# Kernel optimization log

Measured on AMD Instinct MI355X. Metric: run time of the kernel, lower is better.

The kernel has to match this reference:

```python
import jax, jax.numpy as jnp
import numpy as np

EPS = 1e-8  # torch F.cosine_similarity eps
QK_DIM = 16


def conv2d(x, w, b=None):
    # x: [N,C,H,W], w: [O,I,kh,kw]
    y = jax.lax.conv_general_dilated(x, w, (1, 1), 'SAME',
                                     dimension_numbers=('NCHW', 'OIHW', 'NCHW'))
    return y if b is None else y + b[None, :, None, None]


def setup_inputs() -> dict:
    key = jax.random.key(0)
    ks = jax.random.split(key, 32)
    N, H, W = 5, 256, 256
    c_vox, c_feat, c_det, c_sem = 8, 64, 8, 32
    c_total = c_vox + c_feat + c_det  # 80
    r = lambda k, sh: jax.random.normal(k, sh, dtype=jnp.float32)
    p = lambda k, sh: 0.02 * jax.random.normal(k, sh, dtype=jnp.float32)
    return {
        # BEV inputs
        'ego_vox': r(ks[0], (1, c_vox, H, W)),
        'ego_feat': r(ks[1], (1, c_feat, H, W)),
        'ego_det': r(ks[2], (1, c_det, H, W)),
        'collab_vox': r(ks[3], (N, c_vox, H, W)),
        'collab_feat': r(ks[4], (N, c_feat, H, W)),
        'collab_det': r(ks[5], (N, c_det, H, W)),
        # QueryGenerator (1x1 conv, no bias)
        'q_w': p(ks[6], (QK_DIM, c_feat, 1, 1)),
        # Channel_Request_Attention shared MLP (1x1 convs, no bias, ratio=16)
        'ch_w1': p(ks[7], (c_feat // 16, c_feat)),
        'ch_w2': p(ks[8], (c_feat, c_feat // 16)),
        # KeyGenerator (1x1 convs, no bias)
        'k_w1': p(ks[9], (QK_DIM, c_vox, 1, 1)),
        'k_w2': p(ks[10], (QK_DIM, c_feat, 1, 1)),
        'k_w3': p(ks[11], (QK_DIM, c_det, 1, 1)),
        # AttentionGenerator: spatial branch
        'sp_w1': p(ks[12], (64, c_total, 3, 3)), 'sp_b1': jnp.zeros((64,), jnp.float32),
        'sp_w2': p(ks[13], (1, 64, 1, 1)), 'sp_b2': jnp.zeros((1,), jnp.float32),
        # AttentionGenerator: granularity branch (linears)
        'gr_w1': p(ks[14], (32, c_total)), 'gr_b1': jnp.zeros((32,), jnp.float32),
        'gr_w2': p(ks[15], (3, 32)), 'gr_b2': jnp.zeros((3,), jnp.float32),
        # AttentionGenerator: semantic branch
        'se_w1': p(ks[16], (128, c_feat, 3, 3)), 'se_b1': jnp.zeros((128,), jnp.float32),
        'se_w2': p(ks[17], (c_sem, 128, 1, 1)), 'se_b2': jnp.zeros((c_sem,), jnp.float32),
    }


def _forward(ego_vox, ego_feat, ego_det, collab_vox, collab_feat, collab_det,
             q_w, ch_w1, ch_w2, k_w1, k_w2, k_w3,
             sp_w1, sp_b1, sp_w2, sp_b2, gr_w1, gr_b1, gr_w2, gr_b2,
             se_w1, se_b1, se_w2, se_b2):
    N = collab_vox.shape[0]

    # ---- _calculate_contribution(ref=ego broadcast to N, contrib=collab) ----
    # padded cosine sims reduce to slice-dot / (||slice|| * ||ref_full||)
    sq = lambda t: jnp.sum(t * t, axis=1)                      # [*,H,W]
    ref_norm = jnp.sqrt(sq(ego_vox) + sq(ego_feat) + sq(ego_det))  # [1,H,W]
    denom_ref = jnp.maximum(ref_norm, EPS)

    def sim(contrib, ego_part):
        dot = jnp.sum(contrib * ego_part, axis=1)              # [N,H,W]
        n = jnp.maximum(jnp.sqrt(sq(contrib)), EPS)
        return dot / (n * denom_ref)

    contribution = jnp.stack(
        [sim(collab_vox, ego_vox), sim(collab_feat, ego_feat), sim(collab_det, ego_det)],
        axis=1)                                                 # [N,3,H,W]
    contribution = (contribution + 1.0) * 0.5

    # ---- QueryGenerator / KeyGenerator cross-agent attention ----
    q = conv2d(ego_feat, q_w)                                   # [1,16,H,W]
    k1 = conv2d(collab_vox, k_w1)                               # [N,16,H,W]
    k2 = conv2d(collab_feat, k_w2)
    k3 = conv2d(collab_det, k_w3)
    scale = 1.0 / np.sqrt(QK_DIM).astype(np.float32)
    scores = jnp.stack([jnp.sum(q * k, axis=1) for k in (k1, k2, k3)],
                       axis=1) * scale                          # [N,3,H,W]
    qk_attn = jax.nn.softmax(scores, axis=1)

    # ---- Channel_Request_Attention on ego feat (note: max_pool is also avg pool in source) ----
    pooled = jnp.mean(ego_feat, axis=(2, 3))                    # [1,64]
    m = jax.nn.relu(pooled @ ch_w1.T) @ ch_w2.T                 # [1,64]
    channel_attn = jax.nn.sigmoid(m + m)[:, :, None, None]      # [1,64,1,1]

    # ---- AttentionGenerator over collaborators ----
    full = jnp.concatenate([collab_vox, collab_feat, collab_det], axis=1)  # [N,80,H,W]
    spatial_attn = jax.nn.sigmoid(
        conv2d(jax.nn.relu(conv2d(full, sp_w1, sp_b1)), sp_w2, sp_b2))     # [N,1,H,W]
    pooled_full = jnp.mean(full, axis=(2, 3))                   # [N,80]
    gran_attn = jax.nn.softmax(
        jax.nn.relu(pooled_full @ gr_w1.T + gr_b1) @ gr_w2.T + gr_b2,
        axis=-1)[:, :, None, None]                              # [N,3,1,1]
    sem_attn = conv2d(jax.nn.relu(conv2d(collab_feat, se_w1, se_b1)),
                      se_w2, se_b2)                             # [N,32,H,W]

    return (contribution, qk_attn, spatial_attn, gran_attn, sem_attn, channel_attn)


def reference(ego_vox, ego_feat, ego_det, collab_vox, collab_feat, collab_det,
              q_w, ch_w1, ch_w2, k_w1, k_w2, k_w3,
              sp_w1, sp_b1, sp_w2, sp_b2, gr_w1, gr_b1, gr_w2, gr_b2,
              se_w1, se_b1, se_w2, se_b2):
    return _forward(ego_vox, ego_feat, ego_det, collab_vox, collab_feat, collab_det,
                    q_w, ch_w1, ch_w2, k_w1, k_w2, k_w3,
                    sp_w1, sp_b1, sp_w2, sp_b2, gr_w1, gr_b1, gr_w2, gr_b2,
                    se_w1, se_b1, se_w2, se_b2)
```

## Files before the change

kernel.cpp:

```cpp
#include <hip/hip_runtime.h>
#include <math.h>

#define HW 65536
#define NAG 5
#define EPSF 1e-8f

typedef __attribute__((ext_vector_type(8))) short short8;
typedef __attribute__((ext_vector_type(4))) float f32x4;

__device__ __forceinline__ unsigned short f2bf(float f) {
    union { float f; unsigned int u; } v; v.f = f;
    unsigned int r = v.u + 0x7FFF + ((v.u >> 16) & 1);
    return (unsigned short)(r >> 16);
}

__device__ __forceinline__ void gload_lds16(const unsigned short* g, unsigned short* l) {
    __builtin_amdgcn_global_load_lds(
        (__attribute__((address_space(1))) void*)(g),
        (__attribute__((address_space(3))) void*)(l),
        16, 0, 0);
}

__device__ __forceinline__ int swz1280(int orig) {
    return (orig & 7) * 160 + (orig >> 3);
}

__device__ __forceinline__ f32x4 MF(short8 a, short8 b, f32x4 c) {
    return __builtin_amdgcn_mfma_f32_16x16x32_bf16(a, b, c, 0, 0, 0);
}


__global__ __launch_bounds__(256) void k_transpose(
    const float* __restrict__ q_w, const float* __restrict__ k_w1,
    const float* __restrict__ k_w2, const float* __restrict__ k_w3,
    float* __restrict__ qwT, float* __restrict__ kw1T,
    float* __restrict__ kw2T, float* __restrict__ kw3T)
{
    int i = blockIdx.x * 256 + threadIdx.x;
    if (i < 1024)  { int o = i / 64,  c = i % 64;  qwT[c * 16 + o] = q_w[i];
                                                   kw2T[c * 16 + o] = k_w2[i]; }
    if (i < 128)   { int o = i / 8,   c = i % 8;   kw1T[c * 16 + o] = k_w1[i];
                                                   kw3T[c * 16 + o] = k_w3[i]; }
}

__global__ __launch_bounds__(256) void k_prep(
    const float* __restrict__ se_w1, const float* __restrict__ se_w2,
    const float* __restrict__ sp_w1,
    unsigned short* __restrict__ wbf, unsigned short* __restrict__ w2bf,
    unsigned short* __restrict__ wspf, unsigned short* __restrict__ wspv)
{
    int i = blockIdx.x * 256 + threadIdx.x;
    if (i < 73728) {
        int c = i & 63, mid = (i >> 6) & 127, tap = i >> 13;
        wbf[i] = f2bf(se_w1[(mid * 64 + c) * 9 + tap]);
    }
    if (i < 4096) w2bf[i] = f2bf(se_w2[i]);
    if (i < 36864) {
        int c = i & 63, mid = (i >> 6) & 63, tap = i >> 12;
        wspf[i] = f2bf(sp_w1[(mid * 80 + 8 + c) * 9 + tap]);
    }
    if (i < 18432) {
        int c = i & 31, mid = (i >> 5) & 63, tap = i >> 11;
        float v = 0.f;
        if (c < 8)       v = sp_w1[(mid * 80 + c) * 9 + tap];
        else if (c < 16) v = sp_w1[(mid * 80 + 64 + c) * 9 + tap];
        wspv[i] = f2bf(v);
    }
}

__global__ __launch_bounds__(256) void k_prep_nhwc(
    const float* __restrict__ ego_feat,
    const float* __restrict__ collab_vox, const float* __restrict__ collab_feat,
    const float* __restrict__ collab_det,
    unsigned short* __restrict__ featNHWC, unsigned short* __restrict__ vdNHWC,
    float* __restrict__ partials)
{
    __shared__ float lds_f[64 * 65];
    const int y = blockIdx.x, n = blockIdx.y;
    const int t = threadIdx.x;
    const bool ego = (n == 5);
    const float* featsrc = ego ? ego_feat : collab_feat + (size_t)n * 64 * HW;

    float psum = 0.f;
    const int c_ld = t >> 2, q0 = t & 3;
    for (int chunk = 0; chunk < 4; ++chunk) {
        const int x0c = chunk * 64;
        __syncthreads();
#pragma unroll
        for (int q = q0; q < 16; q += 4) {
            float4 v = *(const float4*)&featsrc[(size_t)c_ld * HW + y * 256 + x0c + q * 4];
            lds_f[c_ld * 65 + q * 4 + 0] = v.x;
            lds_f[c_ld * 65 + q * 4 + 1] = v.y;
            lds_f[c_ld * 65 + q * 4 + 2] = v.z;
            lds_f[c_ld * 65 + q * 4 + 3] = v.w;
            psum += (v.x + v.y) + (v.z + v.w);
        }
        __syncthreads();
        if (!ego) {
#pragma unroll
            for (int half = 0; half < 2; ++half) {
                int g = t & 7, xl = (t >> 3) + half * 32;
                int x = x0c + xl;
                int cg = g ^ (x & 7);
                unsigned short pk[8];
#pragma unroll
                for (int i = 0; i < 8; ++i)
                    pk[i] = f2bf(lds_f[(cg * 8 + i) * 65 + xl]);
                *(short8*)&featNHWC[(((size_t)n * 256 + y) * 256 + x) * 64 + g * 8] =
                    *(const short8*)pk;
            }
        }
    }
    psum += __shfl_xor(psum, 1, 64);
    psum += __shfl_xor(psum, 2, 64);
    if (q0 == 0) {
        int row = ego ? c_ld : 64 + n * 80 + 8 + c_ld;
        partials[row * 256 + y] = psum;
    }
    if (ego) return;

    float psv = 0.f;
    const int c2 = t >> 4, q2 = t & 15;
    const float* vdsrc = (c2 < 8) ? collab_vox + ((size_t)n * 8 + c2) * HW
                                  : collab_det + ((size_t)n * 8 + (c2 - 8)) * HW;
    for (int chunk = 0; chunk < 4; ++chunk) {
        const int x0c = chunk * 64;
        __syncthreads();
        {
            float4 v = *(const float4*)&vdsrc[y * 256 + x0c + q2 * 4];
            lds_f[c2 * 65 + q2 * 4 + 0] = v.x;
            lds_f[c2 * 65 + q2 * 4 + 1] = v.y;
            lds_f[c2 * 65 + q2 * 4 + 2] = v.z;
            lds_f[c2 * 65 + q2 * 4 + 3] = v.w;
            psv += (v.x + v.y) + (v.z + v.w);
        }
        __syncthreads();
        {
            int g = t & 3, xl = t >> 2;
            int x = x0c + xl;
            int cg = g ^ (x & 3);
            unsigned short pk[8];
#pragma unroll
            for (int i = 0; i < 8; ++i) {
                int cc = cg * 8 + i;
                pk[i] = (cc < 16) ? f2bf(lds_f[cc * 65 + xl]) : (unsigned short)0;
            }
            *(short8*)&vdNHWC[(((size_t)n * 256 + y) * 256 + x) * 32 + g * 8] =
                *(const short8*)pk;
        }
    }
    psv += __shfl_xor(psv, 1, 64);
    psv += __shfl_xor(psv, 2, 64);
    psv += __shfl_xor(psv, 4, 64);
    psv += __shfl_xor(psv, 8, 64);
    if (q2 == 0) {
        int row = 64 + n * 80 + (c2 < 8 ? c2 : c2 + 64);
        partials[row * 256 + y] = psv;
    }
}

__global__ __launch_bounds__(256) void k_pool2(
    const float* __restrict__ partials, float* __restrict__ pool)
{
    __shared__ float red[256];
    int r = blockIdx.x, t = threadIdx.x;
    red[t] = partials[r * 256 + t];
    __syncthreads();
    for (int s = 128; s > 0; s >>= 1) {
        if (t < s) red[t] += red[t + s];
        __syncthreads();
    }
    if (t == 0) pool[r] = red[0] * (1.f / HW);
}

__global__ __launch_bounds__(256) void k_contrib_qk(
    const float* __restrict__ ego_vox, const float* __restrict__ ego_feat,
    const float* __restrict__ ego_det,
    const float* __restrict__ collab_vox, const float* __restrict__ collab_feat,
    const float* __restrict__ collab_det,
    const float* __restrict__ qw, const float* __restrict__ kw1,
    const float* __restrict__ kw2, const float* __restrict__ kw3,
    float* __restrict__ out_contrib, float* __restrict__ out_qk)
{
    const int n = blockIdx.x >> 8;
    const int p = ((blockIdx.x & 255) << 8) | threadIdx.x;

    float q[16], k2[16];
#pragma unroll
    for (int o = 0; o < 16; o++) { q[o] = 0.f; k2[o] = 0.f; }
    float sq_ref = 0.f, dot_f = 0.f, sq_cf = 0.f;
#pragma unroll 4
    for (int c = 0; c < 64; c++) {
        float e = ego_feat[c * HW + p];
        float x = collab_feat[(n * 64 + c) * HW + p];
        sq_ref = fmaf(e, e, sq_ref);
        dot_f  = fmaf(x, e, dot_f);
        sq_cf  = fmaf(x, x, sq_cf);
#pragma unroll
        for (int o = 0; o < 16; o++) {
            q[o]  = fmaf(qw[c * 16 + o], e, q[o]);
            k2[o] = fmaf(kw2[c * 16 + o], x, k2[o]);
        }
    }
    float kx[16];
#pragma unroll
    for (int o = 0; o < 16; o++) kx[o] = 0.f;
    float dot_v = 0.f, sq_cv = 0.f;
#pragma unroll
    for (int c = 0; c < 8; c++) {
        float e = ego_vox[c * HW + p];
        float x = collab_vox[(n * 8 + c) * HW + p];
        sq_ref = fmaf(e, e, sq_ref);
        dot_v  = fmaf(x, e, dot_v);
        sq_cv  = fmaf(x, x, sq_cv);
#pragma unroll
        for (int o = 0; o < 16; o++)
            kx[o] = fmaf(kw1[c * 16 + o], x, kx[o]);
    }
    float s1 = 0.f;
#pragma unroll
    for (int o = 0; o < 16; o++) s1 = fmaf(q[o], kx[o], s1);
#pragma unroll
    for (int o = 0; o < 16; o++) kx[o] = 0.f;
    float dot_d = 0.f, sq_cd = 0.f;
#pragma unroll
    for (int c = 0; c < 8; c++) {
        float e = ego_det[c * HW + p];
        float x = collab_det[(n * 8 + c) * HW + p];
        sq_ref = fmaf(e, e, sq_ref);
        dot_d  = fmaf(x, e, dot_d);
        sq_cd  = fmaf(x, x, sq_cd);
#pragma unroll
        for (int o = 0; o < 16; o++)
            kx[o] = fmaf(kw3[c * 16 + o], x, kx[o]);
    }
    float s3 = 0.f, s2 = 0.f;
#pragma unroll
    for (int o = 0; o < 16; o++) { s3 = fmaf(q[o], kx[o], s3); s2 = fmaf(q[o], k2[o], s2); }

    float inv_ref = 1.f / fmaxf(sqrtf(sq_ref), EPSF);
    float simv = dot_v / fmaxf(sqrtf(sq_cv), EPSF) * inv_ref;
    float simf = dot_f / fmaxf(sqrtf(sq_cf), EPSF) * inv_ref;
    float simd_ = dot_d / fmaxf(sqrtf(sq_cd), EPSF) * inv_ref;
    out_contrib[(n * 3 + 0) * HW + p] = (simv + 1.f) * 0.5f;
    out_contrib[(n * 3 + 1) * HW + p] = (simf + 1.f) * 0.5f;
    out_contrib[(n * 3 + 2) * HW + p] = (simd_ + 1.f) * 0.5f;

    s1 *= 0.25f; s2 *= 0.25f; s3 *= 0.25f;
    float m = fmaxf(s1, fmaxf(s2, s3));
    float e1 = __expf(s1 - m), e2 = __expf(s2 - m), e3 = __expf(s3 - m);
    float inv = 1.f / (e1 + e2 + e3);
    out_qk[(n * 3 + 0) * HW + p] = e1 * inv;
    out_qk[(n * 3 + 1) * HW + p] = e2 * inv;
    out_qk[(n * 3 + 2) * HW + p] = e3 * inv;
}

__global__ __launch_bounds__(192) void k_mlps(
    const float* __restrict__ pool,
    const float* __restrict__ ch_w1, const float* __restrict__ ch_w2,
    const float* __restrict__ gr_w1, const float* __restrict__ gr_b1,
    const float* __restrict__ gr_w2, const float* __restrict__ gr_b2,
    float* __restrict__ out_gran, float* __restrict__ out_chan)
{
    __shared__ float h4[4], h32[5][32], logit[5][3];
    int t = threadIdx.x;
    if (t < 4) {
        float a = 0.f;
        for (int c = 0; c < 64; c++) a = fmaf(ch_w1[t * 64 + c], pool[c], a);
        h4[t] = fmaxf(a, 0.f);
    }
    if (t < 160) {
        int n = t >> 5, i = t & 31;
        float a = gr_b1[i];
        for (int c = 0; c < 80; c++) a = fmaf(gr_w1[i * 80 + c], pool[64 + n * 80 + c], a);
        h32[n][i] = fmaxf(a, 0.f);
    }
    __syncthreads();
    if (t < 64) {
        float m = 0.f;
#pragma unroll
        for (int j = 0; j < 4; j++) m = fmaf(ch_w2[t * 4 + j], h4[j], m);
        out_chan[t] = 1.f / (1.f + __expf(-2.f * m));
    }
    if (t < 15) {
        int n = t / 3, j = t % 3;
        float a = gr_b2[j];
#pragma unroll
        for (int i = 0; i < 32; i++) a = fmaf(gr_w2[j * 32 + i], h32[n][i], a);
        logit[n][j] = a;
    }
    __syncthreads();
    if (t < 5) {
        float a = logit[t][0], b = logit[t][1], c = logit[t][2];
        float m = fmaxf(a, fmaxf(b, c));
        float ea = __expf(a - m), eb = __expf(b - m), ec = __expf(c - m);
        float inv = 1.f / (ea + eb + ec);
        out_gran[t * 3 + 0] = ea * inv;
        out_gran[t * 3 + 1] = eb * inv;
        out_gran[t * 3 + 2] = ec * inv;
    }
}

__global__ __launch_bounds__(512, 4) void k_sem_nhwc(
    const unsigned short* __restrict__ featNHWC,
    const unsigned short* __restrict__ wbf,
    const unsigned short* __restrict__ w2bf,
    const float* __restrict__ se_b1, const float* __restrict__ se_b2,
    float* __restrict__ out_sem)
{
    __shared__ __align__(16) unsigned short smem[256 * 128];
    const int bid = swz1280((int)blockIdx.x);
    const int n = bid >> 8, rem = bid & 255;
    const int x0 = (rem & 3) << 6, y0 = (rem >> 2) << 2;
    const int tid = threadIdx.x, lane = tid & 63, w = tid >> 6;
    const int wr = w >> 1, wc = w & 1;
    const int l15 = lane & 15, lg = lane >> 4;
    const short8 z8 = {0, 0, 0, 0, 0, 0, 0, 0};

    if (y0 == 0)
        for (int i = tid; i < 528; i += 512) *(short8*)&smem[i * 8] = z8;
    if (y0 == 252)
        for (int i = tid; i < 528; i += 512) *(short8*)&smem[5 * 66 * 64 + i * 8] = z8;

    for (int idx = w; idx < 48; idx += 8) {
        int dy = idx >> 3, k = idx & 7, gy = y0 - 1 + dy;
        if ((unsigned)gy < 256u)
            gload_lds16(
                &featNHWC[(((size_t)n * 256 + gy) * 256 + x0 + k * 8 + (lane >> 3)) * 64 + (lane & 7) * 8],
                &smem[(dy * 66 + 1 + k * 8) * 64]);
    }
    if (tid < 96) {
        int dy = tid >> 4, rem2 = tid & 15, side = rem2 >> 3, c8 = rem2 & 7;
        int gy = y0 - 1 + dy, gx = side ? x0 + 64 : x0 - 1, col = side ? 65 : 0;
        short8 v = z8;
        if ((unsigned)gy < 256u && (unsigned)gx < 256u)
            v = *(const short8*)&featNHWC[(((size_t)n * 256 + gy) * 256 + gx) * 64 + c8 * 8];
        *(short8*)&smem[(dy * 66 + col) * 64 + c8 * 8] = v;
    }
    __syncthreads();

    const int midb = wc * 64 + l15;
    f32x4 acc[4][4] = {};
    short8 bc[4], bn[4];
#pragma unroll
    for (int nf = 0; nf < 4; ++nf)
        bc[nf] = *(const short8*)&wbf[(0 * 128 + midb + nf * 16) * 64 + lg * 8];

#pragma unroll 1
    for (int p = 0; p < 18; ++p) {
        const int tap = p >> 1, kc = p & 1;
        const int dyrow = tap / 3, dx = tap % 3;
        const int pn = (p < 17) ? p + 1 : 17;
        const int tapn = pn >> 1, kcn = pn & 1;
#pragma unroll
        for (int nf = 0; nf < 4; ++nf)
            bn[nf] = *(const short8*)&wbf[(tapn * 128 + midb + nf * 16) * 64 + kcn * 32 + lg * 8];
        const int c0 = kc * 32 + lg * 8;
        const int dyb = (wr + dyrow) * 66;
        short8 a[4];
#pragma unroll
        for (int mf = 0; mf < 4; ++mf) {
            int col = mf * 16 + l15 + dx;
            a[mf] = *(const short8*)&smem[(dyb + col) * 64 + (c0 ^ (((col + 7) & 7) << 3))];
        }
        __builtin_amdgcn_s_setprio(1);
#pragma unroll
        for (int mf = 0; mf < 4; ++mf)
#pragma unroll
            for (int nf = 0; nf < 4; ++nf)
                acc[mf][nf] = MF(a[mf], bc[nf], acc[mf][nf]);
        __builtin_amdgcn_s_setprio(0);
#pragma unroll
        for (int nf = 0; nf < 4; ++nf) bc[nf] = bn[nf];
    }
    __syncthreads();

#pragma unroll
    for (int nf = 0; nf < 4; ++nf) {
        int mid = wc * 64 + nf * 16 + l15;
        float b1 = se_b1[mid];
#pragma unroll
        for (int mf = 0; mf < 4; ++mf) {
            int mrow = wr * 64 + mf * 16 + lg * 4;
#pragma unroll
            for (int rr = 0; rr < 4; ++rr) {
                int m = mrow + rr;
                float v = fmaxf(acc[mf][nf][rr] + b1, 0.f);
                smem[m * 128 + (mid ^ ((m & 7) << 3))] = f2bf(v);
            }
        }
    }
    __syncthreads();

    f32x4 acc2[2][2] = {};
    const int pxb = w * 32;
#pragma unroll
    for (int kc = 0; kc < 4; ++kc) {
        const int k0 = kc * 32 + lg * 8;
        short8 a2[2], b2[2];
#pragma unroll
        for (int mf = 0; mf < 2; ++mf) {
            int m = pxb + mf * 16 + l15;
            a2[mf] = *(const short8*)&smem[m * 128 + (k0 ^ ((m & 7) << 3))];
        }
#pragma unroll
        for (int nf = 0; nf < 2; ++nf) {
            int j = nf * 16 + l15;
            b2[nf] = *(const short8*)&w2bf[j * 128 + k0];
        }
#pragma unroll
        for (int mf = 0; mf < 2; ++mf)
#pragma unroll
            for (int nf = 0; nf < 2; ++nf)
                acc2[mf][nf] = MF(a2[mf], b2[nf], acc2[mf][nf]);
    }
#pragma unroll
    for (int nf = 0; nf < 2; ++nf) {
        int j = nf * 16 + l15;
        float bj = se_b2[j];
#pragma unroll
        for (int mf = 0; mf < 2; ++mf) {
            int m = pxb + mf * 16 + lg * 4;
            int oy = m >> 6, x = m & 63;
            float4 v;
            v.x = acc2[mf][nf][0] + bj; v.y = acc2[mf][nf][1] + bj;
            v.z = acc2[mf][nf][2] + bj; v.w = acc2[mf][nf][3] + bj;
            *(float4*)&out_sem[(size_t)(n * 32 + j) * HW + (y0 + oy) * 256 + x0 + x] = v;
        }
    }
}

__global__ __launch_bounds__(512, 4) void k_spatial_nhwc(
    const unsigned short* __restrict__ featNHWC,
    const unsigned short* __restrict__ vdNHWC,
    const unsigned short* __restrict__ wspf,
    const unsigned short* __restrict__ wspv,
    const float* __restrict__ sp_b1, const float* __restrict__ sp_w2,
    const float* __restrict__ sp_b2,
    float* __restrict__ out_sp)
{
    __shared__ __align__(16) unsigned short sF[6 * 66 * 64];
    __shared__ __align__(16) unsigned short sV[6 * 66 * 32];
    const int bid = swz1280((int)blockIdx.x);
    const int n = bid >> 8, rem = bid & 255;
    const int x0 = (rem & 3) << 6, y0 = (rem >> 2) << 2;
    const int tid = threadIdx.x, lane = tid & 63, w = tid >> 6;
    const int l15 = lane & 15, lg = lane >> 4;
    const int wr = w >> 1, wc = w & 1;
    const short8 z8 = {0, 0, 0, 0, 0, 0, 0, 0};

    if (y0 == 0) {
        for (int i = tid; i < 528; i += 512) *(short8*)&sF[i * 8] = z8;
        for (int i = tid; i < 264; i += 512) *(short8*)&sV[i * 8] = z8;
    }
    if (y0 == 252) {
        for (int i = tid; i < 528; i += 512) *(short8*)&sF[5 * 66 * 64 + i * 8] = z8;
        for (int i = tid; i < 264; i += 512) *(short8*)&sV[5 * 66 * 32 + i * 8] = z8;
    }
    for (int idx = w; idx < 48; idx += 8) {
        int dy = idx >> 3, k = idx & 7, gy = y0 - 1 + dy;
        if ((unsigned)gy < 256u)
            gload_lds16(
                &featNHWC[(((size_t)n * 256 + gy) * 256 + x0 + k * 8 + (lane >> 3)) * 64 + (lane & 7) * 8],
                &sF[(dy * 66 + 1 + k * 8) * 64]);
    }
    for (int idx = w; idx < 24; idx += 8) {
        int dy = idx >> 2, k = idx & 3, gy = y0 - 1 + dy;
        if ((unsigned)gy < 256u)
            gload_lds16(
                &vdNHWC[(((size_t)n * 256 + gy) * 256 + x0 + k * 16 + (lane >> 2)) * 32 + (lane & 3) * 8],
                &sV[(dy * 66 + 1 + k * 16) * 32]);
    }
    if (tid < 96) {
        int dy = tid >> 4, rem2 = tid & 15, side = rem2 >> 3, c8 = rem2 & 7;
        int gy = y0 - 1 + dy, gx = side ? x0 + 64 : x0 - 1, col = side ? 65 : 0;
        short8 v = z8;
        if ((unsigned)gy < 256u && (unsigned)gx < 256u)
            v = *(const short8*)&featNHWC[(((size_t)n * 256 + gy) * 256 + gx) * 64 + c8 * 8];
        *(short8*)&sF[(dy * 66 + col) * 64 + c8 * 8] = v;
    } else if (tid < 144) {
        int t2 = tid - 96;
        int dy = t2 >> 3, rem2 = t2 & 7, side = rem2 >> 2, g4 = rem2 & 3;
        int gy = y0 - 1 + dy, gx = side ? x0 + 64 : x0 - 1, col = side ? 65 : 0;
        short8 v = z8;
        if ((unsigned)gy < 256u && (unsigned)gx < 256u)
            v = *(const short8*)&vdNHWC[(((size_t)n * 256 + gy) * 256 + gx) * 32 + g4 * 8];
        *(short8*)&sV[(dy * 66 + col) * 32 + g4 * 8] = v;
    }
    __syncthreads();

    f32x4 acc[4][2] = {};
    const int mid0 = wc * 32 + l15, mid1 = wc * 32 + 16 + l15;

    short8 bc0 = *(const short8*)&wspf[(0 * 64 + mid0) * 64 + lg * 8];
    short8 bc1 = *(const short8*)&wspf[(0 * 64 + mid1) * 64 + lg * 8];
#pragma unroll 1
    for (int p = 0; p < 18; ++p) {
        const int tap = p >> 1, kc = p & 1;
        const int dyrow = tap / 3, dx = tap % 3;
        const int pn = (p < 17) ? p + 1 : 17;
        const int tapn = pn >> 1, kcn = pn & 1;
        short8 bn0 = *(const short8*)&wspf[(tapn * 64 + mid0) * 64 + kcn * 32 + lg * 8];
        short8 bn1 = *(const short8*)&wspf[(tapn * 64 + mid1) * 64 + kcn * 32 + lg * 8];
        const int c0 = kc * 32 + lg * 8;
        const int dyb = (wr + dyrow) * 66;
        short8 a[4];
#pragma unroll
        for (int mf = 0; mf < 4; ++mf) {
            int col = mf * 16 + l15 + dx;
            a[mf] = *(const short8*)&sF[(dyb + col) * 64 + (c0 ^ (((col + 7) & 7) << 3))];
        }
        __builtin_amdgcn_s_setprio(1);
#pragma unroll
        for (int mf = 0; mf < 4; ++mf) {
            acc[mf][0] = MF(a[mf], bc0, acc[mf][0]);
            acc[mf][1] = MF(a[mf], bc1, acc[mf][1]);
        }
        __builtin_amdgcn_s_setprio(0);
        bc0 = bn0; bc1 = bn1;
    }

    const int c0v = lg * 8;
    short8 vc0 = *(const short8*)&wspv[(0 * 64 + mid0) * 32 + c0v];
    short8 vc1 = *(const short8*)&wspv[(0 * 64 + mid1) * 32 + c0v];
#pragma unroll 1
    for (int tap = 0; tap < 9; ++tap) {
        const int dyrow = tap / 3, dx = tap % 3;
        const int tapn = (tap < 8) ? tap + 1 : 8;
        short8 vn0 = *(const short8*)&wspv[(tapn * 64 + mid0) * 32 + c0v];
        short8 vn1 = *(const short8*)&wspv[(tapn * 64 + mid1) * 32 + c0v];
        const int dyb = (wr + dyrow) * 66;
        short8 a[4];
#pragma unroll
        for (int mf = 0; mf < 4; ++mf) {
            int col = mf * 16 + l15 + dx;
            a[mf] = *(const short8*)&sV[(dyb + col) * 32 + (c0v ^ (((col + 3) & 3) << 3))];
        }
        __builtin_amdgcn_s_setprio(1);
#pragma unroll
        for (int mf = 0; mf < 4; ++mf) {
            acc[mf][0] = MF(a[mf], vc0, acc[mf][0]);
            acc[mf][1] = MF(a[mf], vc1, acc[mf][1]);
        }
        __builtin_amdgcn_s_setprio(0);
        vc0 = vn0; vc1 = vn1;
    }

    const float w2v0 = sp_w2[mid0], w2v1 = sp_w2[mid1];
    const float b1v0 = sp_b1[mid0], b1v1 = sp_b1[mid1];
    float4 part[4];
#pragma unroll
    for (int mf = 0; mf < 4; ++mf) {
#pragma unroll
        for (int rr = 0; rr < 4; ++rr) {
            float s = fmaf(w2v0, fmaxf(acc[mf][0][rr] + b1v0, 0.f),
                           w2v1 * fmaxf(acc[mf][1][rr] + b1v1, 0.f));
            s += __shfl_xor(s, 1, 64);
            s += __shfl_xor(s, 2, 64);
            s += __shfl_xor(s, 4, 64);
            s += __shfl_xor(s, 8, 64);
            ((float*)&part[mf])[rr] = s;
        }
    }
    __syncthreads();
    float4* sP = (float4*)sV;
    if (wc == 1 && l15 == 0) {
#pragma unroll
        for (int mf = 0; mf < 4; ++mf) sP[(wr * 4 + mf) * 4 + lg] = part[mf];
    }
    __syncthreads();
    if (wc == 0 && l15 == 0) {
        const float b2 = sp_b2[0];
#pragma unroll
        for (int mf = 0; mf < 4; ++mf) {
            float4 o = sP[(wr * 4 + mf) * 4 + lg];
            float4 vout;
            vout.x = 1.f / (1.f + __expf(-(part[mf].x + o.x + b2)));
            vout.y = 1.f / (1.f + __expf(-(part[mf].y + o.y + b2)));
            vout.z = 1.f / (1.f + __expf(-(part[mf].z + o.z + b2)));
            vout.w = 1.f / (1.f + __expf(-(part[mf].w + o.w + b2)));
            *(float4*)&out_sp[(size_t)n * HW + (y0 + wr) * 256 + x0 + mf * 16 + lg * 4] = vout;
        }
    }
}

extern "C" void kernel_launch(void* const* d_in, const int* in_sizes, int n_in,
                              void* d_out, int out_size, void* d_ws, size_t ws_size,
                              hipStream_t stream)
{
    (void)in_sizes; (void)n_in; (void)out_size; (void)ws_size;
    const float* ego_vox     = (const float*)d_in[0];
    const float* ego_feat    = (const float*)d_in[1];
    const float* ego_det     = (const float*)d_in[2];
    const float* collab_vox  = (const float*)d_in[3];
    const float* collab_feat = (const float*)d_in[4];
    const float* collab_det  = (const float*)d_in[5];
    const float* q_w   = (const float*)d_in[6];
    const float* ch_w1 = (const float*)d_in[7];
    const float* ch_w2 = (const float*)d_in[8];
    const float* k_w1  = (const float*)d_in[9];
    const float* k_w2  = (const float*)d_in[10];
    const float* k_w3  = (const float*)d_in[11];
    const float* sp_w1 = (const float*)d_in[12];
    const float* sp_b1 = (const float*)d_in[13];
    const float* sp_w2 = (const float*)d_in[14];
    const float* sp_b2 = (const float*)d_in[15];
    const float* gr_w1 = (const float*)d_in[16];
    const float* gr_b1 = (const float*)d_in[17];
    const float* gr_w2 = (const float*)d_in[18];
    const float* gr_b2 = (const float*)d_in[19];
    const float* se_w1 = (const float*)d_in[20];
    const float* se_b1 = (const float*)d_in[21];
    const float* se_w2 = (const float*)d_in[22];
    const float* se_b2 = (const float*)d_in[23];

    float* out = (float*)d_out;
    float* o_contrib = out;
    float* o_qk      = out + 983040;
    float* o_sp      = out + 1966080;
    float* o_gran    = out + 2293760;
    float* o_sem     = out + 2293775;
    float* o_chan    = out + 12779535;

    float* wsf  = (float*)d_ws;
    float* pool = wsf;
    float* qwT  = wsf + 464;
    float* kw1T = wsf + 1488;
    float* kw2T = wsf + 1616;
    float* kw3T = wsf + 2640;
    unsigned short* wbf  = (unsigned short*)(wsf + 122576);
    unsigned short* w2bf = (unsigned short*)(wsf + 159440);
    unsigned short* wspf = (unsigned short*)(wsf + 161488);
    unsigned short* wspv = (unsigned short*)(wsf + 179920);
    unsigned short* featNHWC = (unsigned short*)(wsf + 189136);
    unsigned short* vdNHWC   = (unsigned short*)(wsf + 10674896);
    float* partials          = wsf + 15917776;

    k_prep<<<288, 256, 0, stream>>>(se_w1, se_w2, sp_w1, wbf, w2bf, wspf, wspv);
    k_transpose<<<4, 256, 0, stream>>>(q_w, k_w1, k_w2, k_w3, qwT, kw1T, kw2T, kw3T);

    k_contrib_qk<<<1280, 256, 0, stream>>>(
        ego_vox, ego_feat, ego_det, collab_vox, collab_feat, collab_det,
        qwT, kw1T, kw2T, kw3T, o_contrib, o_qk);

    k_prep_nhwc<<<dim3(256, 6), 256, 0, stream>>>(
        ego_feat, collab_vox, collab_feat, collab_det,
        featNHWC, vdNHWC, partials);
    k_pool2<<<464, 256, 0, stream>>>(partials, pool);
    k_mlps<<<1, 192, 0, stream>>>(pool, ch_w1, ch_w2, gr_w1, gr_b1, gr_w2, gr_b2,
                                  o_gran, o_chan);

    k_spatial_nhwc<<<1280, 512, 0, stream>>>(
        featNHWC, vdNHWC, wspf, wspv, sp_b1, sp_w2, sp_b2, o_sp);
    k_sem_nhwc<<<1280, 512, 0, stream>>>(
        featNHWC, wbf, w2bf, se_b1, se_b2, o_sem);
}
```

Measured before the change: 255.5 us.

## Halve semantic-conv LDS footprint by staging hidden activations in two passes

The semantic branch kernel now sizes its shared buffer to the input halo tile (6x66x64) rather than the full 256x128 hidden tile. The ReLU'd hidden activations are written and consumed in two halves of 128 pixels each, with an extra barrier between halves, and the launch bound occupancy hint goes from 4 to 6. The aim is to cut LDS per block so more blocks fit per CU and latency is hidden better. The cost is an extra synchronization round and less parallel second-GEMM work per wave.

```diff
diff --git a/kernel.cpp b/kernel.cpp
--- a/kernel.cpp
+++ b/kernel.cpp
@@ -301,14 +301,14 @@
     }
 }
 
-__global__ __launch_bounds__(512, 4) void k_sem_nhwc(
+__global__ __launch_bounds__(512, 6) void k_sem_nhwc(
     const unsigned short* __restrict__ featNHWC,
     const unsigned short* __restrict__ wbf,
     const unsigned short* __restrict__ w2bf,
     const float* __restrict__ se_b1, const float* __restrict__ se_b2,
     float* __restrict__ out_sem)
 {
-    __shared__ __align__(16) unsigned short smem[256 * 128];
+    __shared__ __align__(16) unsigned short smem[6 * 66 * 64];
     const int bid = swz1280((int)blockIdx.x);
     const int n = bid >> 8, rem = bid & 255;
     const int x0 = (rem & 3) << 6, y0 = (rem >> 2) << 2;
@@ -375,58 +375,57 @@
     }
     __syncthreads();
 
-#pragma unroll
-    for (int nf = 0; nf < 4; ++nf) {
-        int mid = wc * 64 + nf * 16 + l15;
-        float b1 = se_b1[mid];
-#pragma unroll
-        for (int mf = 0; mf < 4; ++mf) {
-            int mrow = wr * 64 + mf * 16 + lg * 4;
-#pragma unroll
-            for (int rr = 0; rr < 4; ++rr) {
-                int m = mrow + rr;
-                float v = fmaxf(acc[mf][nf][rr] + b1, 0.f);
-                smem[m * 128 + (mid ^ ((m & 7) << 3))] = f2bf(v);
+#pragma unroll 1
+    for (int h = 0; h < 2; ++h) {
+        if ((wr >> 1) == h) {
+            const int rbase = (wr & 1) * 64;
+#pragma unroll
+            for (int nf = 0; nf < 4; ++nf) {
+                int mid = wc * 64 + nf * 16 + l15;
+                float b1 = se_b1[mid];
+#pragma unroll
+                for (int mf = 0; mf < 4; ++mf) {
+                    int mrow = rbase + mf * 16 + lg * 4;
+#pragma unroll
+                    for (int rr = 0; rr < 4; ++rr) {
+                        int m = mrow + rr;
+                        float v = fmaxf(acc[mf][nf][rr] + b1, 0.f);
+                        smem[m * 128 + (mid ^ ((m & 7) << 3))] = f2bf(v);
+                    }
+                }
             }
         }
-    }
-    __syncthreads();
-
-    f32x4 acc2[2][2] = {};
-    const int pxb = w * 32;
-#pragma unroll
-    for (int kc = 0; kc < 4; ++kc) {
-        const int k0 = kc * 32 + lg * 8;
-        short8 a2[2], b2[2];
-#pragma unroll
-        for (int mf = 0; mf < 2; ++mf) {
-            int m = pxb + mf * 16 + l15;
-            a2[mf] = *(const short8*)&smem[m * 128 + (k0 ^ ((m & 7) << 3))];
+        __syncthreads();
+
+        f32x4 acc2[2] = {};
+        const int pxb = w * 16;
+#pragma unroll
+        for (int kc = 0; kc < 4; ++kc) {
+            const int k0 = kc * 32 + lg * 8;
+            int m = pxb + l15;
+            short8 a2 = *(const short8*)&smem[m * 128 + (k0 ^ ((m & 7) << 3))];
+            short8 b2[2];
+#pragma unroll
+            for (int nf = 0; nf < 2; ++nf) {
+                int j = nf * 16 + l15;
+                b2[nf] = *(const short8*)&w2bf[j * 128 + k0];
+            }
+#pragma unroll
+            for (int nf = 0; nf < 2; ++nf)
+                acc2[nf] = MF(a2, b2[nf], acc2[nf]);
         }
 #pragma unroll
         for (int nf = 0; nf < 2; ++nf) {
             int j = nf * 16 + l15;
-            b2[nf] = *(const short8*)&w2bf[j * 128 + k0];
-        }
-#pragma unroll
-        for (int mf = 0; mf < 2; ++mf)
-#pragma unroll
-            for (int nf = 0; nf < 2; ++nf)
-                acc2[mf][nf] = MF(a2[mf], b2[nf], acc2[mf][nf]);
-    }
-#pragma unroll
-    for (int nf = 0; nf < 2; ++nf) {
-        int j = nf * 16 + l15;
-        float bj = se_b2[j];
-#pragma unroll
-        for (int mf = 0; mf < 2; ++mf) {
-            int m = pxb + mf * 16 + lg * 4;
-            int oy = m >> 6, x = m & 63;
+            float bj = se_b2[j];
+            int m = pxb + lg * 4;
+            int oy = h * 2 + (m >> 6), x = m & 63;
             float4 v;
-            v.x = acc2[mf][nf][0] + bj; v.y = acc2[mf][nf][1] + bj;
-            v.z = acc2[mf][nf][2] + bj; v.w = acc2[mf][nf][3] + bj;
+            v.x = acc2[nf][0] + bj; v.y = acc2[nf][1] + bj;
+            v.z = acc2[nf][2] + bj; v.w = acc2[nf][3] + bj;
             *(float4*)&out_sem[(size_t)(n * 32 + j) * HW + (y0 + oy) * 256 + x0 + x] = v;
         }
+        if (h == 0) __syncthreads();
     }
 }
 
```

New measurement: 973.4 us. 3.81x slower.
